# Performance work log

Hardware: AMD Instinct MI355X
Metric: run time of the kernel (lower is better)

## Reference

```python
import jax, jax.numpy as jnp
import numpy as np

N_NODES = 100000
N_EDGES = 1600000
D_FEAT = 256
HIDDEN = 256
N_CLASSES = 64


def gcn_conv(x, edge_index, W, b, num_nodes):
    """PyG GCNConv: h = W x; add self loops; symmetric D^-1/2 (A+I) D^-1/2 aggregation; + bias."""
    h = x @ W  # [N, out]
    loop = jnp.arange(num_nodes, dtype=edge_index.dtype)
    row = jnp.concatenate([edge_index[0], loop])  # source nodes
    col = jnp.concatenate([edge_index[1], loop])  # target nodes
    deg = jax.ops.segment_sum(jnp.ones_like(col, dtype=h.dtype), col, num_segments=num_nodes)
    dinv = jnp.where(deg > 0, jax.lax.rsqrt(deg), 0.0)
    norm = dinv[row] * dinv[col]  # per-edge normalization
    out = jax.ops.segment_sum(h[row] * norm[:, None], col, num_segments=num_nodes)
    return out + b


def setup_inputs() -> dict:
    key = jax.random.key(0)
    k1, k2, k3, k4 = jax.random.split(key, 4)
    x = jax.random.normal(k1, (N_NODES, D_FEAT), dtype=jnp.float32)
    edge_index = jax.random.randint(k2, (2, N_EDGES), 0, N_NODES, dtype=jnp.int64)
    W1 = jax.random.normal(k3, (D_FEAT, HIDDEN), dtype=jnp.float32) * (1.0 / np.sqrt(D_FEAT))
    b1 = jnp.zeros((HIDDEN,), dtype=jnp.float32)
    W2 = jax.random.normal(k4, (HIDDEN, N_CLASSES), dtype=jnp.float32) * (1.0 / np.sqrt(HIDDEN))
    b2 = jnp.zeros((N_CLASSES,), dtype=jnp.float32)
    return {"x": x, "edge_index": edge_index, "W1": W1, "b1": b1, "W2": W2, "b2": b2}


def reference(x, edge_index, W1, b1, W2, b2):
    # conv1 -> relu -> dropout (eval mode: identity) -> conv2
    h = gcn_conv(x, edge_index, W1, b1, N_NODES)
    h = jax.nn.relu(h)
    out = gcn_conv(h, edge_index, W2, b2, N_NODES)  # [N, num_classes]
    return out
```

## Files before the change

### kernel.cpp

```cpp
#include <hip/hip_runtime.h>
#include <hip/hip_bf16.h>

#define N_NODES 100000
#define N_PAD   100032
#define N_EDGES 1600000
#define D_FEAT 256
#define HIDDEN 256
#define N_CLASSES 64

#define NBKT 391
#define TILE 4096
#define CAP  8192

typedef __attribute__((ext_vector_type(8))) short bf16x8;
typedef __attribute__((ext_vector_type(4))) float f32x4;

__device__ inline float b2f(ushort u) {
    unsigned v = ((unsigned)u) << 16;
    float f; __builtin_memcpy(&f, &v, 4); return f;
}
__device__ inline ushort f2b(float f) {
    unsigned u; __builtin_memcpy(&u, &f, 4);
    unsigned r = (u + 0x7fffu + ((u >> 16) & 1u)) >> 16;
    return (ushort)r;
}

__global__ __launch_bounds__(256)
void zero_bcnt(int* bcnt) {
    int i = blockIdx.x * 256 + threadIdx.x;
    if (i < NBKT) bcnt[i] = 0;
}

__global__ __launch_bounds__(256)
void bin_count(const int* __restrict__ cols, int* bcnt, int nE) {
    __shared__ int h[NBKT];
    int t = threadIdx.x;
    for (int i = t; i < NBKT; i += 256) h[i] = 0;
    __syncthreads();
    for (long e = (long)blockIdx.x * 256 + t; e < nE; e += (long)gridDim.x * 256)
        atomicAdd(&h[cols[e] >> 8], 1);
    __syncthreads();
    for (int i = t; i < NBKT; i += 256)
        if (h[i]) atomicAdd(&bcnt[i], h[i]);
}

__global__ __launch_bounds__(256)
void bucket_scan(const int* __restrict__ bcnt, int* __restrict__ bbase,
                 int* __restrict__ bcur, int* __restrict__ offsets) {
    __shared__ int sd[256];
    int t = threadIdx.x;
    int i0 = 2 * t, i1 = 2 * t + 1;
    int a = (i0 < NBKT) ? bcnt[i0] : 0;
    int b = (i1 < NBKT) ? bcnt[i1] : 0;
    int s = a + b;
    sd[t] = s; __syncthreads();
    #pragma unroll
    for (int off = 1; off < 256; off <<= 1) {
        int v = (t >= off) ? sd[t - off] : 0;
        __syncthreads();
        sd[t] += v;
        __syncthreads();
    }
    int ex = sd[t] - s;
    if (i0 <= NBKT) bbase[i0] = ex;
    if (i0 < NBKT)  bcur[i0] = ex;
    if (i1 <= NBKT) bbase[i1] = ex + a;
    if (i1 < NBKT)  bcur[i1] = ex + a;
    if (t == 0) offsets[N_NODES] = N_EDGES;
}

__global__ __launch_bounds__(256)
void bin_scatter(const int* __restrict__ rows, const int* __restrict__ cols,
                 int* bcur, unsigned* __restrict__ bins, int nE)
{
    __shared__ unsigned recs[TILE];
    __shared__ ushort bos[TILE];
    __shared__ int hist[NBKT], excl[NBKT], cursor[NBKT], gbase[NBKT];
    __shared__ int sd[256];
    int t = threadIdx.x;
    long e0 = (long)blockIdx.x * TILE;
    int cnt = (int)min((long)TILE, (long)nE - e0);
    for (int i = t; i < NBKT; i += 256) hist[i] = 0;
    __syncthreads();
    int myrow[TILE / 256], mycol[TILE / 256];
    #pragma unroll
    for (int k = 0; k < TILE / 256; ++k) {
        int i = k * 256 + t;
        if (i < cnt) {
            myrow[k] = rows[e0 + i];
            mycol[k] = cols[e0 + i];
            atomicAdd(&hist[mycol[k] >> 8], 1);
        }
    }
    __syncthreads();
    {
        int i0 = 2 * t, i1 = 2 * t + 1;
        int a = (i0 < NBKT) ? hist[i0] : 0;
        int b = (i1 < NBKT) ? hist[i1] : 0;
        int s = a + b;
        sd[t] = s; __syncthreads();
        #pragma unroll
        for (int off = 1; off < 256; off <<= 1) {
            int v = (t >= off) ? sd[t - off] : 0;
            __syncthreads();
            sd[t] += v;
            __syncthreads();
        }
        int ex = sd[t] - s;
        if (i0 < NBKT) { excl[i0] = ex;     cursor[i0] = ex; }
        if (i1 < NBKT) { excl[i1] = ex + a; cursor[i1] = ex + a; }
    }
    __syncthreads();
    #pragma unroll
    for (int k = 0; k < TILE / 256; ++k) {
        int i = k * 256 + t;
        if (i < cnt) {
            int b = mycol[k] >> 8;
            int s = atomicAdd(&cursor[b], 1);
            recs[s] = ((unsigned)(mycol[k] & 255) << 24) | (unsigned)myrow[k];
            bos[s] = (ushort)b;
        }
    }
    __syncthreads();
    for (int i = t; i < NBKT; i += 256)
        if (hist[i] > 0) gbase[i] = atomicAdd(&bcur[i], hist[i]);
    __syncthreads();
    for (int i = t; i < cnt; i += 256) {
        int b = bos[i];
        bins[gbase[b] + (i - excl[b])] = recs[i];
    }
}

__global__ __launch_bounds__(256)
void bucket_fill(const unsigned* __restrict__ bins, const int* __restrict__ bbase,
                 int* __restrict__ offsets, float* __restrict__ dinv,
                 int* __restrict__ esrc)
{
    int b = blockIdx.x, t = threadIdx.x;
    int s0 = bbase[b], s1 = bbase[b + 1];
    int len = s1 - s0;
    __shared__ int cnt[256];
    __shared__ int sd[256];
    __shared__ int cur[256];
    __shared__ int stage[CAP];
    cnt[t] = 0;
    __syncthreads();
    for (int i = t; i < len; i += 256) atomicAdd(&cnt[bins[s0 + i] >> 24], 1);
    __syncthreads();
    int c = cnt[t];
    sd[t] = c; __syncthreads();
    #pragma unroll
    for (int off = 1; off < 256; off <<= 1) {
        int v = (t >= off) ? sd[t - off] : 0;
        __syncthreads();
        sd[t] += v;
        __syncthreads();
    }
    int ex = sd[t] - c;
    cur[t] = ex;
    int node = b * 256 + t;
    if (node < N_NODES) {
        offsets[node] = s0 + ex;
        dinv[node] = rsqrtf(1.0f + (float)c);
    }
    __syncthreads();
    if (len <= CAP) {
        for (int i = t; i < len; i += 256) {
            unsigned r = bins[s0 + i];
            int p = atomicAdd(&cur[r >> 24], 1);
            stage[p] = (int)(r & 0xFFFFFFu);
        }
        __syncthreads();
        for (int i = t; i < len; i += 256) esrc[s0 + i] = stage[i];
    } else {
        for (int i = t; i < len; i += 256) {
            unsigned r = bins[s0 + i];
            int p = atomicAdd(&cur[r >> 24], 1);
            esrc[s0 + p] = (int)(r & 0xFFFFFFu);
        }
    }
}

__global__ __launch_bounds__(256)
void split_x(const float* __restrict__ x, ushort* __restrict__ xh, ushort* __restrict__ xl) {
    int i = blockIdx.x * 256 + threadIdx.x;
    if (i >= N_NODES * D_FEAT / 4) return;
    float4 v = ((const float4*)x)[i];
    ushort4 h, l;
    h.x = f2b(v.x); l.x = f2b(v.x - b2f(h.x));
    h.y = f2b(v.y); l.y = f2b(v.y - b2f(h.y));
    h.z = f2b(v.z); l.z = f2b(v.z - b2f(h.z));
    h.w = f2b(v.w); l.w = f2b(v.w - b2f(h.w));
    ((ushort4*)xh)[i] = h;
    ((ushort4*)xl)[i] = l;
}

__global__ __launch_bounds__(256)
void fragw1(const float* __restrict__ W1, ushort* __restrict__ wfh, ushort* __restrict__ wfl) {
    int t = blockIdx.x * 256 + threadIdx.x;
    int ks = t >> 10, nb = (t >> 6) & 15, lane = t & 63;
    int m = lane & 15, quad = lane >> 4;
    ushort h8[8], l8[8];
    #pragma unroll
    for (int j = 0; j < 8; ++j) {
        int k = ks * 32 + quad * 8 + j;
        float w = W1[k * HIDDEN + nb * 16 + m];
        h8[j] = f2b(w);
        l8[j] = f2b(w - b2f(h8[j]));
    }
    long off = ((long)(ks * 16 + nb) * 64 + lane) * 8;
    *(ushort4*)&wfh[off]     = make_ushort4(h8[0], h8[1], h8[2], h8[3]);
    *(ushort4*)&wfh[off + 4] = make_ushort4(h8[4], h8[5], h8[6], h8[7]);
    *(ushort4*)&wfl[off]     = make_ushort4(l8[0], l8[1], l8[2], l8[3]);
    *(ushort4*)&wfl[off + 4] = make_ushort4(l8[4], l8[5], l8[6], l8[7]);
}

__global__ __launch_bounds__(256)
void fragw2(const float* __restrict__ W2, ushort* __restrict__ wf) {
    int t = blockIdx.x * 256 + threadIdx.x;
    int ks = t >> 8, nb = (t >> 6) & 3, lane = t & 63;
    int m = lane & 15, quad = lane >> 4;
    ushort h8[8];
    #pragma unroll
    for (int j = 0; j < 8; ++j) {
        int k = ks * 32 + quad * 8 + j;
        h8[j] = f2b(W2[k * N_CLASSES + nb * 16 + m]);
    }
    long off = ((long)(ks * 4 + nb) * 64 + lane) * 8;
    *(ushort4*)&wf[off]     = make_ushort4(h8[0], h8[1], h8[2], h8[3]);
    *(ushort4*)&wf[off + 4] = make_ushort4(h8[4], h8[5], h8[6], h8[7]);
}

__global__ __launch_bounds__(256)
void gemm1_mfma(const ushort* __restrict__ xh, const ushort* __restrict__ xl,
                const ushort* __restrict__ wfh, const ushort* __restrict__ wfl,
                const float* __restrict__ dinv, ushort* __restrict__ hs)
{
    int tid = threadIdx.x;
    int wm = tid >> 6, lane = tid & 63;
    int row0 = blockIdx.x * 64 + wm * 16;
    int m = lane & 15, quad = lane >> 4;
    long arow = row0 + m;

    f32x4 acc[16];
    #pragma unroll
    for (int nb = 0; nb < 16; ++nb) acc[nb] = (f32x4){0.f, 0.f, 0.f, 0.f};

    const ushort* aph = xh + arow * D_FEAT + quad * 8;
    const ushort* apl = xl + arow * D_FEAT + quad * 8;

    for (int ks = 0; ks < 8; ++ks) {
        bf16x8 ah = *(const bf16x8*)(aph + ks * 32);
        bf16x8 al = *(const bf16x8*)(apl + ks * 32);
        const ushort* bh = wfh + ((long)(ks * 16) * 64 + lane) * 8;
        const ushort* bl = wfl + ((long)(ks * 16) * 64 + lane) * 8;
        #pragma unroll
        for (int nb = 0; nb < 16; ++nb) {
            bf16x8 wbh = *(const bf16x8*)(bh + (long)nb * 64 * 8);
            bf16x8 wbl = *(const bf16x8*)(bl + (long)nb * 64 * 8);
            acc[nb] = __builtin_amdgcn_mfma_f32_16x16x32_bf16(ah, wbh, acc[nb], 0, 0, 0);
            acc[nb] = __builtin_amdgcn_mfma_f32_16x16x32_bf16(ah, wbl, acc[nb], 0, 0, 0);
            acc[nb] = __builtin_amdgcn_mfma_f32_16x16x32_bf16(al, wbh, acc[nb], 0, 0, 0);
        }
    }

    #pragma unroll
    for (int reg = 0; reg < 4; ++reg) {
        int row = row0 + quad * 4 + reg;
        if (row < N_NODES) {
            float dv = dinv[row];
            #pragma unroll
            for (int nb = 0; nb < 16; ++nb)
                hs[(long)row * HIDDEN + nb * 16 + m] = f2b(acc[nb][reg] * dv);
        }
    }
}

__global__ __launch_bounds__(256)
void gemm2_mfma(const ushort* __restrict__ r1s, const ushort* __restrict__ wf,
                ushort* __restrict__ h2)
{
    int tid = threadIdx.x;
    int wm = tid >> 6, lane = tid & 63;
    int row0 = blockIdx.x * 64 + wm * 16;
    int m = lane & 15, quad = lane >> 4;
    long arow = row0 + m;

    f32x4 acc[4];
    #pragma unroll
    for (int nb = 0; nb < 4; ++nb) acc[nb] = (f32x4){0.f, 0.f, 0.f, 0.f};

    const ushort* ap = r1s + arow * HIDDEN + quad * 8;

    for (int ks = 0; ks < 8; ++ks) {
        bf16x8 a = *(const bf16x8*)(ap + ks * 32);
        const ushort* bp = wf + ((long)(ks * 4) * 64 + lane) * 8;
        #pragma unroll
        for (int nb = 0; nb < 4; ++nb) {
            bf16x8 b = *(const bf16x8*)(bp + (long)nb * 64 * 8);
            acc[nb] = __builtin_amdgcn_mfma_f32_16x16x32_bf16(a, b, acc[nb], 0, 0, 0);
        }
    }

    #pragma unroll
    for (int reg = 0; reg < 4; ++reg) {
        int row = row0 + quad * 4 + reg;
        if (row < N_NODES) {
            #pragma unroll
            for (int nb = 0; nb < 4; ++nb)
                h2[(long)row * N_CLASSES + nb * 16 + m] = f2b(acc[nb][reg]);
        }
    }
}

__global__ __launch_bounds__(256)
void agg256(const ushort* __restrict__ src, const int* __restrict__ offsets,
            const int* __restrict__ esrc, const float* __restrict__ dinv,
            const float* __restrict__ b1, ushort* __restrict__ dst)
{
    int wave = threadIdx.x >> 6, lane = threadIdx.x & 63;
    int v = blockIdx.x * 4 + wave;
    int c = lane << 2;
    ushort4 s = *(const ushort4*)&src[(long)v * 256 + c];
    float a0 = b2f(s.x), a1 = b2f(s.y), a2 = b2f(s.z), a3 = b2f(s.w);
    int e = offsets[v], end = offsets[v + 1];
    for (; e + 4 <= end; e += 4) {
        int s0 = esrc[e], s1 = esrc[e + 1], s2 = esrc[e + 2], s3 = esrc[e + 3];
        ushort4 u0 = *(const ushort4*)&src[(long)s0 * 256 + c];
        ushort4 u1 = *(const ushort4*)&src[(long)s1 * 256 + c];
        ushort4 u2 = *(const ushort4*)&src[(long)s2 * 256 + c];
        ushort4 u3 = *(const ushort4*)&src[(long)s3 * 256 + c];
        a0 += (b2f(u0.x) + b2f(u1.x)) + (b2f(u2.x) + b2f(u3.x));
        a1 += (b2f(u0.y) + b2f(u1.y)) + (b2f(u2.y) + b2f(u3.y));
        a2 += (b2f(u0.z) + b2f(u1.z)) + (b2f(u2.z) + b2f(u3.z));
        a3 += (b2f(u0.w) + b2f(u1.w)) + (b2f(u2.w) + b2f(u3.w));
    }
    for (; e < end; ++e) {
        ushort4 u = *(const ushort4*)&src[(long)esrc[e] * 256 + c];
        a0 += b2f(u.x); a1 += b2f(u.y); a2 += b2f(u.z); a3 += b2f(u.w);
    }
    float dv = dinv[v];
    float4 bb = *(const float4*)&b1[c];
    float r0 = dv * fmaxf(fmaf(dv, a0, bb.x), 0.f);
    float r1 = dv * fmaxf(fmaf(dv, a1, bb.y), 0.f);
    float r2 = dv * fmaxf(fmaf(dv, a2, bb.z), 0.f);
    float r3 = dv * fmaxf(fmaf(dv, a3, bb.w), 0.f);
    *(ushort4*)&dst[(long)v * 256 + c] = make_ushort4(f2b(r0), f2b(r1), f2b(r2), f2b(r3));
}

__global__ __launch_bounds__(256)
void agg64b(const ushort* __restrict__ src, const int* __restrict__ offsets,
            const int* __restrict__ esrc, const float* __restrict__ dinv,
            const float* __restrict__ b2, float* __restrict__ out)
{
    int wave = threadIdx.x >> 6, lane = threadIdx.x & 63;
    int v = blockIdx.x * 4 + wave;
    float acc = b2f(src[(long)v * 64 + lane]);
    int e = offsets[v], end = offsets[v + 1];
    for (; e + 4 <= end; e += 4) {
        int s0 = esrc[e], s1 = esrc[e + 1], s2 = esrc[e + 2], s3 = esrc[e + 3];
        float a0 = b2f(src[(long)s0 * 64 + lane]);
        float a1 = b2f(src[(long)s1 * 64 + lane]);
        float a2 = b2f(src[(long)s2 * 64 + lane]);
        float a3 = b2f(src[(long)s3 * 64 + lane]);
        acc += (a0 + a1) + (a2 + a3);
    }
    for (; e < end; ++e) acc += b2f(src[(long)esrc[e] * 64 + lane]);
    out[(long)v * 64 + lane] = fmaf(dinv[v], acc, b2[lane]);
}

#define WS_DINV   0UL
#define WS_OFFS   524288UL
#define WS_BCNT   1048576UL
#define WS_BBASE  1052672UL
#define WS_BCUR   1056768UL
#define WS_ESRC   1064960UL
#define WS_BINS   7602176UL
#define WS_XH     20447232UL
#define WS_XL     71663616UL
#define WS_WF1H   122880000UL
#define WS_WF1L   123011072UL
#define WS_WF2    123142144UL
#define WS_HS1    123174912UL

extern "C" void kernel_launch(void* const* d_in, const int* in_sizes, int n_in,
                              void* d_out, int out_size, void* d_ws, size_t ws_size,
                              hipStream_t stream)
{
    const float* x  = (const float*)d_in[0];
    const int*   ei = (const int*)d_in[1];
    const float* W1 = (const float*)d_in[2];
    const float* b1 = (const float*)d_in[3];
    const float* W2 = (const float*)d_in[4];
    const float* b2 = (const float*)d_in[5];
    float* out = (float*)d_out;

    const int* rows = ei;
    const int* cols = ei + N_EDGES;

    char* ws = (char*)d_ws;
    float*    dinv    = (float*)(ws + WS_DINV);
    int*      offsets = (int*)(ws + WS_OFFS);
    int*      bcnt    = (int*)(ws + WS_BCNT);
    int*      bbase   = (int*)(ws + WS_BBASE);
    int*      bcur    = (int*)(ws + WS_BCUR);
    int*      esrc    = (int*)(ws + WS_ESRC);
    unsigned* bins    = (unsigned*)(ws + WS_BINS);
    ushort*   xh      = (ushort*)(ws + WS_XH);
    ushort*   xl      = (ushort*)(ws + WS_XL);
    ushort*   wf1h    = (ushort*)(ws + WS_WF1H);
    ushort*   wf1l    = (ushort*)(ws + WS_WF1L);
    ushort*   wf2     = (ushort*)(ws + WS_WF2);
    ushort*   hs1     = (ushort*)(ws + WS_HS1);
    ushort*   r1s     = xl;
    ushort*   h2      = xh;

    zero_bcnt<<<2, 256, 0, stream>>>(bcnt);
    bin_count<<<512, 256, 0, stream>>>(cols, bcnt, N_EDGES);
    bucket_scan<<<1, 256, 0, stream>>>(bcnt, bbase, bcur, offsets);
    bin_scatter<<<(N_EDGES + TILE - 1) / TILE, 256, 0, stream>>>(rows, cols, bcur, bins, N_EDGES);
    bucket_fill<<<NBKT, 256, 0, stream>>>(bins, bbase, offsets, dinv, esrc);

    split_x<<<(N_NODES * D_FEAT / 4 + 255) / 256, 256, 0, stream>>>(x, xh, xl);
    fragw1<<<32, 256, 0, stream>>>(W1, wf1h, wf1l);
    fragw2<<<8, 256, 0, stream>>>(W2, wf2);

    const int gemm_grid = (N_NODES + 63) / 64;
    const int agg_grid  = N_NODES / 4;

    gemm1_mfma<<<gemm_grid, 256, 0, stream>>>(xh, xl, wf1h, wf1l, dinv, hs1);
    agg256<<<agg_grid, 256, 0, stream>>>(hs1, offsets, esrc, dinv, b1, r1s);

    gemm2_mfma<<<gemm_grid, 256, 0, stream>>>(r1s, wf2, h2);
    agg64b<<<agg_grid, 256, 0, stream>>>(h2, offsets, esrc, dinv, b2, out);
}
```

Baseline: 525.8 us.

## Retile MFMA GEMMs so each wave computes a 64x64 output block

Both GEMM kernels are retiled so that each wave computes four 16-row M fragments instead of one. Each loaded B fragment is then reused across four A fragments. GEMM1 now uses a 2D grid that splits the 256 output columns into two halves, with waves covering a 2x2 layout. GEMM2 gives each block 256 rows. This cuts redundant weight-fragment loads from global memory and raises MFMA work per load, at the cost of more accumulator registers and fewer blocks. Rows past N_NODES are read beyond the valid range, which relies on the padded buffers.

```diff
diff --git a/kernel.cpp b/kernel.cpp
--- a/kernel.cpp
+++ b/kernel.cpp
@@ -237,43 +237,53 @@
                 const float* __restrict__ dinv, ushort* __restrict__ hs)
 {
     int tid = threadIdx.x;
-    int wm = tid >> 6, lane = tid & 63;
-    int row0 = blockIdx.x * 64 + wm * 16;
+    int lane = tid & 63;
+    int wm = (tid >> 6) & 1;
+    int wn = tid >> 7;
+    int row0 = blockIdx.y * 128 + wm * 64;
+    int nb0 = blockIdx.x * 8 + wn * 4;
     int m = lane & 15, quad = lane >> 4;
-    long arow = row0 + m;
-
-    f32x4 acc[16];
-    #pragma unroll
-    for (int nb = 0; nb < 16; ++nb) acc[nb] = (f32x4){0.f, 0.f, 0.f, 0.f};
-
-    const ushort* aph = xh + arow * D_FEAT + quad * 8;
-    const ushort* apl = xl + arow * D_FEAT + quad * 8;
+
+    f32x4 acc[4][4];
+    #pragma unroll
+    for (int i = 0; i < 4; ++i)
+        #pragma unroll
+        for (int j = 0; j < 4; ++j) acc[i][j] = (f32x4){0.f, 0.f, 0.f, 0.f};
 
     for (int ks = 0; ks < 8; ++ks) {
-        bf16x8 ah = *(const bf16x8*)(aph + ks * 32);
-        bf16x8 al = *(const bf16x8*)(apl + ks * 32);
-        const ushort* bh = wfh + ((long)(ks * 16) * 64 + lane) * 8;
-        const ushort* bl = wfl + ((long)(ks * 16) * 64 + lane) * 8;
-        #pragma unroll
-        for (int nb = 0; nb < 16; ++nb) {
-            bf16x8 wbh = *(const bf16x8*)(bh + (long)nb * 64 * 8);
-            bf16x8 wbl = *(const bf16x8*)(bl + (long)nb * 64 * 8);
-            acc[nb] = __builtin_amdgcn_mfma_f32_16x16x32_bf16(ah, wbh, acc[nb], 0, 0, 0);
-            acc[nb] = __builtin_amdgcn_mfma_f32_16x16x32_bf16(ah, wbl, acc[nb], 0, 0, 0);
-            acc[nb] = __builtin_amdgcn_mfma_f32_16x16x32_bf16(al, wbh, acc[nb], 0, 0, 0);
-        }
-    }
-
-    #pragma unroll
-    for (int reg = 0; reg < 4; ++reg) {
-        int row = row0 + quad * 4 + reg;
-        if (row < N_NODES) {
-            float dv = dinv[row];
+        bf16x8 ah[4], al[4];
+        #pragma unroll
+        for (int mf = 0; mf < 4; ++mf) {
+            long r = (long)(row0 + mf * 16 + m);
+            ah[mf] = *(const bf16x8*)(xh + r * D_FEAT + ks * 32 + quad * 8);
+            al[mf] = *(const bf16x8*)(xl + r * D_FEAT + ks * 32 + quad * 8);
+        }
+        #pragma unroll
+        for (int nbl = 0; nbl < 4; ++nbl) {
+            long boff = ((long)(ks * 16 + nb0 + nbl) * 64 + lane) * 8;
+            bf16x8 bh = *(const bf16x8*)(wfh + boff);
+            bf16x8 bl = *(const bf16x8*)(wfl + boff);
             #pragma unroll
-            for (int nb = 0; nb < 16; ++nb)
-                hs[(long)row * HIDDEN + nb * 16 + m] = f2b(acc[nb][reg] * dv);
-        }
-    }
+            for (int mf = 0; mf < 4; ++mf) {
+                acc[mf][nbl] = __builtin_amdgcn_mfma_f32_16x16x32_bf16(ah[mf], bh, acc[mf][nbl], 0, 0, 0);
+                acc[mf][nbl] = __builtin_amdgcn_mfma_f32_16x16x32_bf16(ah[mf], bl, acc[mf][nbl], 0, 0, 0);
+                acc[mf][nbl] = __builtin_amdgcn_mfma_f32_16x16x32_bf16(al[mf], bh, acc[mf][nbl], 0, 0, 0);
+            }
+        }
+    }
+
+    #pragma unroll
+    for (int mf = 0; mf < 4; ++mf)
+        #pragma unroll
+        for (int reg = 0; reg < 4; ++reg) {
+            int row = row0 + mf * 16 + quad * 4 + reg;
+            if (row < N_NODES) {
+                float dv = dinv[row];
+                #pragma unroll
+                for (int nbl = 0; nbl < 4; ++nbl)
+                    hs[(long)row * HIDDEN + (nb0 + nbl) * 16 + m] = f2b(acc[mf][nbl][reg] * dv);
+            }
+        }
 }
 
 __global__ __launch_bounds__(256)
@@ -281,36 +291,43 @@
                 ushort* __restrict__ h2)
 {
     int tid = threadIdx.x;
-    int wm = tid >> 6, lane = tid & 63;
-    int row0 = blockIdx.x * 64 + wm * 16;
+    int wv = tid >> 6, lane = tid & 63;
+    int row0 = blockIdx.x * 256 + wv * 64;
     int m = lane & 15, quad = lane >> 4;
-    long arow = row0 + m;
-
-    f32x4 acc[4];
-    #pragma unroll
-    for (int nb = 0; nb < 4; ++nb) acc[nb] = (f32x4){0.f, 0.f, 0.f, 0.f};
-
-    const ushort* ap = r1s + arow * HIDDEN + quad * 8;
+
+    f32x4 acc[4][4];
+    #pragma unroll
+    for (int i = 0; i < 4; ++i)
+        #pragma unroll
+        for (int j = 0; j < 4; ++j) acc[i][j] = (f32x4){0.f, 0.f, 0.f, 0.f};
 
     for (int ks = 0; ks < 8; ++ks) {
-        bf16x8 a = *(const bf16x8*)(ap + ks * 32);
-        const ushort* bp = wf + ((long)(ks * 4) * 64 + lane) * 8;
+        bf16x8 a[4];
+        #pragma unroll
+        for (int mf = 0; mf < 4; ++mf) {
+            long r = (long)(row0 + mf * 16 + m);
+            a[mf] = *(const bf16x8*)(r1s + r * HIDDEN + ks * 32 + quad * 8);
+        }
         #pragma unroll
         for (int nb = 0; nb < 4; ++nb) {
-            bf16x8 b = *(const bf16x8*)(bp + (long)nb * 64 * 8);
-            acc[nb] = __builtin_amdgcn_mfma_f32_16x16x32_bf16(a, b, acc[nb], 0, 0, 0);
-        }
-    }
-
-    #pragma unroll
-    for (int reg = 0; reg < 4; ++reg) {
-        int row = row0 + quad * 4 + reg;
-        if (row < N_NODES) {
+            bf16x8 b = *(const bf16x8*)(wf + ((long)(ks * 4 + nb) * 64 + lane) * 8);
             #pragma unroll
-            for (int nb = 0; nb < 4; ++nb)
-                h2[(long)row * N_CLASSES + nb * 16 + m] = f2b(acc[nb][reg]);
-        }
-    }
+            for (int mf = 0; mf < 4; ++mf)
+                acc[mf][nb] = __builtin_amdgcn_mfma_f32_16x16x32_bf16(a[mf], b, acc[mf][nb], 0, 0, 0);
+        }
+    }
+
+    #pragma unroll
+    for (int mf = 0; mf < 4; ++mf)
+        #pragma unroll
+        for (int reg = 0; reg < 4; ++reg) {
+            int row = row0 + mf * 16 + quad * 4 + reg;
+            if (row < N_NODES) {
+                #pragma unroll
+                for (int nb = 0; nb < 4; ++nb)
+                    h2[(long)row * N_CLASSES + nb * 16 + m] = f2b(acc[mf][nb][reg]);
+            }
+        }
 }
 
 __global__ __launch_bounds__(256)
@@ -425,12 +442,14 @@
     fragw1<<<32, 256, 0, stream>>>(W1, wf1h, wf1l);
     fragw2<<<8, 256, 0, stream>>>(W2, wf2);
 
-    const int gemm_grid = (N_NODES + 63) / 64;
-    const int agg_grid  = N_NODES / 4;
-
-    gemm1_mfma<<<gemm_grid, 256, 0, stream>>>(xh, xl, wf1h, wf1l, dinv, hs1);
+    const int agg_grid = N_NODES / 4;
+
+    {
+        dim3 g1(2, (N_NODES + 127) / 128);
+        gemm1_mfma<<<g1, 256, 0, stream>>>(xh, xl, wf1h, wf1l, dinv, hs1);
+    }
     agg256<<<agg_grid, 256, 0, stream>>>(hs1, offsets, esrc, dinv, b1, r1s);
 
-    gemm2_mfma<<<gemm_grid, 256, 0, stream>>>(r1s, wf2, h2);
+    gemm2_mfma<<<(N_NODES + 255) / 256, 256, 0, stream>>>(r1s, wf2, h2);
     agg64b<<<agg_grid, 256, 0, stream>>>(h2, offsets, esrc, dinv, b2, out);
 }
```

New measurement: 511.7 us. 1.03x faster.
